# Kernel tuning notes

Measured on AMD Instinct MI355X. Metric: run time of the kernel, lower is better.

The kernel has to match this reference:

```python
import jax, jax.numpy as jnp
import numpy as np

B, NQ, T, C = 16, 1024, 2048, 4
DIM, CDIM, H, DH = 512, 256, 1, 128
INNER = H * DH


def _rotate_half(x):
    # pairs interleaved: (..., d*2) -> (-x_odd, x_even) interleaved, matching einops '(d r)' with r=2
    x2 = x.reshape(x.shape[:-1] + (-1, 2))
    a, b = x2[..., 0], x2[..., 1]
    return jnp.stack((-b, a), axis=-1).reshape(x.shape)


def _apply_rotary(freqs, x):
    # freqs: (b, n, d) -> broadcast over heads; x: (b, h, n, d)
    f = freqs[:, None, :, :]
    return x * jnp.cos(f) + _rotate_half(x) * jnp.sin(f)


def _layernorm(x, w, b, eps=1e-5):
    mu = jnp.mean(x, axis=-1, keepdims=True)
    var = jnp.var(x, axis=-1, keepdims=True)
    return (x - mu) * jax.lax.rsqrt(var + eps) * w + b


def setup_inputs() -> dict:
    key = jax.random.key(0)
    ks = jax.random.split(key, 8)
    return dict(
        x_query=jax.random.normal(ks[0], (NQ, DIM), jnp.float32),
        x_context=jax.random.normal(ks[1], (B, T, C, CDIM), jnp.float32),
        rotary_time_emb_query=jax.random.normal(ks[2], (B, NQ, DH), jnp.float32),
        rotary_time_emb_context=jax.random.normal(ks[3], (B, T * C, DH), jnp.float32),
        context_mask=jax.random.randint(ks[4], (B, T), 0, 2) > 0,
        ln_q_w=jnp.ones((DIM,), jnp.float32), ln_q_b=jnp.zeros((DIM,), jnp.float32),
        ln_c_w=jnp.ones((CDIM,), jnp.float32), ln_c_b=jnp.zeros((CDIM,), jnp.float32),
        w_q=jax.random.normal(ks[5], (INNER, DIM), jnp.float32) / np.float32(np.sqrt(DIM)),
        w_kv=jax.random.normal(ks[6], (2 * INNER, CDIM), jnp.float32) / np.float32(np.sqrt(CDIM)),
        w_o=jax.random.normal(ks[7], (DIM, INNER), jnp.float32) / np.float32(np.sqrt(INNER)),
        b_o=jnp.zeros((DIM,), jnp.float32),
    )


def reference(x_query, x_context, rotary_time_emb_query, rotary_time_emb_context,
              context_mask, ln_q_w, ln_q_b, ln_c_w, ln_c_b, w_q, w_kv, w_o, b_o):
    b = x_context.shape[0]
    xq = _layernorm(x_query, ln_q_w, ln_q_b)                      # (NQ, DIM)
    xc = _layernorm(x_context, ln_c_w, ln_c_b)                    # (B, T, C, CDIM)
    q = xq @ w_q.T                                                # (NQ, INNER)
    q = jnp.broadcast_to(q[None], (b,) + q.shape)                 # (B, NQ, INNER)
    kv = xc @ w_kv.T                                              # (B, T, C, 2*INNER)
    k, v = jnp.split(kv, 2, axis=-1)
    k = k.reshape(b, -1, k.shape[-1])                             # (B, T*C, INNER)
    v = v.reshape(b, -1, v.shape[-1])

    def to_heads(t):  # 'b n (h d) -> b h n d'
        return t.reshape(t.shape[0], t.shape[1], H, DH).transpose(0, 2, 1, 3)

    q, k, v = to_heads(q), to_heads(k), to_heads(v)
    q = _apply_rotary(rotary_time_emb_query, q)
    k = _apply_rotary(rotary_time_emb_context, k)
    v = _apply_rotary(rotary_time_emb_context, v)                 # rotate_value=True

    # kv_mask: 'b n -> b 1 1 n' then tiled x4 along last dim (as in source)
    mask = jnp.tile(context_mask[:, None, None, :], (1, 1, 1, 4)) # (B,1,1,4T)
    scale = np.float32(1.0 / np.sqrt(DH))
    logits = jnp.einsum('bhqd,bhkd->bhqk', q, k) * scale
    logits = jnp.where(mask, logits, jnp.float32(-1e30))
    attn = jax.nn.softmax(logits, axis=-1)
    out = jnp.einsum('bhqk,bhkd->bhqd', attn, v)                  # (B,H,NQ,DH)
    out = _apply_rotary(-rotary_time_emb_query, out)              # un-rotate values
    out = out.mean(axis=2)                                        # (B, H, DH)
    return out @ w_o.T + b_o                                      # (B, H, DIM)
```

## Files before the change

kernel.cpp:

```cpp
#include <hip/hip_runtime.h>
#include <hip/hip_bf16.h>


#define DEV static __device__ __forceinline__

typedef __attribute__((ext_vector_type(4))) float f32x4;
typedef __attribute__((ext_vector_type(8))) short s16x8;
typedef __attribute__((ext_vector_type(4))) unsigned u32x4;

constexpr int NB   = 16;
constexpr int NQ   = 1024;
constexpr int SC   = 8192;
constexpr int DIM  = 512;
constexpr int CDIM = 256;
constexpr int DH   = 128;
constexpr int VTR  = 144;
constexpr int VTILE = VTR*64;

DEV short f2bf(float x){
  unsigned u = __builtin_bit_cast(unsigned, x);
  unsigned r = (u + 0x7FFFu + ((u >> 16) & 1u)) >> 16;
  return (short)r;
}

DEV unsigned pk2(float a, float b){
  unsigned short ua = __builtin_bit_cast(unsigned short, __float2bfloat16(a));
  unsigned short ub = __builtin_bit_cast(unsigned short, __float2bfloat16(b));
  return (unsigned)ua | ((unsigned)ub << 16);
}

DEV f32x4 mfma16(s16x8 a, s16x8 b, f32x4 c){
  return __builtin_amdgcn_mfma_f32_16x16x32_bf16(a, b, c, 0, 0, 0);
}

DEV void gload16(const void* g, void* l){
  __builtin_amdgcn_global_load_lds(
      (const __attribute__((address_space(1))) void*)g,
      (__attribute__((address_space(3))) void*)l, 16, 0, 0);
}

DEV s16x8 pexch(int ia0, int ia1, bool hi, unsigned L0, unsigned H0, unsigned L1, unsigned H1){
  int aL0 = __builtin_amdgcn_ds_bpermute(ia0, (int)L0);
  int aL1 = __builtin_amdgcn_ds_bpermute(ia0, (int)L1);
  int aH0 = __builtin_amdgcn_ds_bpermute(ia0, (int)H0);
  int aH1 = __builtin_amdgcn_ds_bpermute(ia0, (int)H1);
  int bL0 = __builtin_amdgcn_ds_bpermute(ia1, (int)L0);
  int bL1 = __builtin_amdgcn_ds_bpermute(ia1, (int)L1);
  int bH0 = __builtin_amdgcn_ds_bpermute(ia1, (int)H0);
  int bH1 = __builtin_amdgcn_ds_bpermute(ia1, (int)H1);
  u32x4 r;
  r[0] = (unsigned)(hi ? aL1 : aL0);
  r[1] = (unsigned)(hi ? aH1 : aH0);
  r[2] = (unsigned)(hi ? bL1 : bL0);
  r[3] = (unsigned)(hi ? bH1 : bH0);
  return __builtin_bit_cast(s16x8, r);
}

__global__ void k_cvtw(const float* __restrict__ wq, const float* __restrict__ wkv,
                       short* __restrict__ wqb, short* __restrict__ wkvb){
  int i = blockIdx.x * 256 + threadIdx.x;
  if(i < 128*512) wqb[i]  = f2bf(wq[i]);
  if(i < 256*256) wkvb[i] = f2bf(wkv[i]);
}

__global__ void k_mask(const unsigned char* __restrict__ raw, unsigned* __restrict__ bits){
  const int b = blockIdx.x, t = threadIdx.x;
  int nz = 0;
  for(int i = t; i < 8192; i += 256){
    unsigned w = ((const unsigned*)raw)[i];
    if(w & 0xFFFFFF00u) nz = 1;
  }
  int any = __syncthreads_or(nz);
  bool isInt = (any == 0);
  if(t < 64){
    unsigned out = 0;
    if(isInt){
      const int* p = (const int*)raw + (b*2048 + t*32);
      for(int j = 0; j < 32; j++) out |= (unsigned)(p[j] != 0) << j;
    } else {
      const unsigned char* p = raw + (b*2048 + t*32);
      for(int j = 0; j < 32; j++) out |= (unsigned)(p[j] != 0) << j;
    }
    bits[b*64 + t] = out;
  }
}

__global__ void k_vrow(const unsigned* __restrict__ bits, short* __restrict__ Vt){
  int b = blockIdx.y;
  int s = blockIdx.x * 256 + threadIdx.x;
  unsigned w = bits[b*64 + ((s & 2047) >> 5)];
  short v = ((w >> (s & 31)) & 1u) ? (short)0x3F80 : (short)0;
  Vt[(((size_t)b*128 + (s >> 6))*VTR + 128)*64 + (s & 63)] = v;
}

__global__ __launch_bounds__(256) void k_stats(const float* __restrict__ xc,
                                               float* __restrict__ MU, float* __restrict__ RS){
  const size_t row = (size_t)blockIdx.x * 16 + (threadIdx.x >> 4);
  const int cl = (threadIdx.x & 15) * 16;
  const float* rp = xc + row * CDIM + cl;
  float s = 0.f, sq = 0.f;
  #pragma unroll
  for(int i = 0; i < 4; i++){
    f32x4 a = *(const f32x4*)(rp + i*4);
    #pragma unroll
    for(int j = 0; j < 4; j++){ s += a[j]; sq += a[j]*a[j]; }
  }
  #pragma unroll
  for(int o = 8; o > 0; o >>= 1){ s += __shfl_xor(s, o); sq += __shfl_xor(sq, o); }
  if((threadIdx.x & 15) == 0){
    float m = s * (1.f/CDIM);
    MU[row] = m;
    RS[row] = rsqrtf(sq * (1.f/CDIM) - m*m + 1e-5f);
  }
}

__global__ __launch_bounds__(256) void k_qproj(const float* __restrict__ xq,
                                               const float* __restrict__ lnw, const float* __restrict__ lnb,
                                               const short* __restrict__ wqb, float* __restrict__ Q0){
  const int wid = threadIdx.x >> 6, lane = threadIdx.x & 63;
  const int g = lane >> 4, li = lane & 15;
  const int row0 = blockIdx.x * 64 + wid * 16;

  float mean = 0.f, rstd = 0.f;
  #pragma unroll
  for(int r = 0; r < 16; r++){
    const float* rp = xq + (row0 + r) * DIM;
    f32x4 a = *(const f32x4*)(rp + lane*8);
    f32x4 b = *(const f32x4*)(rp + lane*8 + 4);
    float s = 0.f, sq = 0.f;
    #pragma unroll
    for(int i = 0; i < 4; i++){ s += a[i] + b[i]; sq += a[i]*a[i] + b[i]*b[i]; }
    #pragma unroll
    for(int o = 32; o > 0; o >>= 1){ s += __shfl_xor(s, o); sq += __shfl_xor(sq, o); }
    if(li == r){
      mean = s / DIM;
      float var = sq / DIM - mean*mean;
      rstd = rsqrtf(var + 1e-5f);
    }
  }

  f32x4 acc[8];
  #pragma unroll
  for(int n = 0; n < 8; n++) acc[n] = f32x4{0.f,0.f,0.f,0.f};

  for(int kc = 0; kc < 16; kc++){
    int kd = kc*32 + g*8;
    const float* rp = xq + (row0 + li)*DIM + kd;
    f32x4 a0 = *(const f32x4*)rp;
    f32x4 a1 = *(const f32x4*)(rp + 4);
    f32x4 w0 = *(const f32x4*)(lnw + kd), w1 = *(const f32x4*)(lnw + kd + 4);
    f32x4 b0 = *(const f32x4*)(lnb + kd), b1 = *(const f32x4*)(lnb + kd + 4);
    s16x8 af;
    #pragma unroll
    for(int i = 0; i < 4; i++){
      af[i]   = f2bf((a0[i] - mean)*rstd*w0[i] + b0[i]);
      af[i+4] = f2bf((a1[i] - mean)*rstd*w1[i] + b1[i]);
    }
    #pragma unroll
    for(int n = 0; n < 8; n++){
      s16x8 bf = *(const s16x8*)(wqb + (n*16 + li)*DIM + kd);
      acc[n] = mfma16(af, bf, acc[n]);
    }
  }
  #pragma unroll
  for(int n = 0; n < 8; n++)
    #pragma unroll
    for(int r = 0; r < 4; r++){
      int m = row0 + g*4 + r;
      Q0[m*DH + n*16 + li] = acc[n][r];
    }
}

__global__ __launch_bounds__(256) void k_kvproj(const float* __restrict__ xc,
                                                const float* __restrict__ lnw, const float* __restrict__ lnb,
                                                const short* __restrict__ wkvb, const float* __restrict__ rc,
                                                const unsigned* __restrict__ bits,
                                                const float* __restrict__ MU, const float* __restrict__ RS,
                                                short* __restrict__ Kd, short* __restrict__ Vt){
  __shared__ __align__(16) short Klds[128][136];
  __shared__ __align__(16) short Vtlds[128][136];
  const int wid = threadIdx.x >> 6, lane = threadIdx.x & 63;
  const int g = lane >> 4, li = lane & 15;
  const int b = blockIdx.y;
  const int s0 = blockIdx.x * 128;
  const int ws0 = s0 + wid * 32;

  float mean_s[2], rstd_s[2];
  #pragma unroll
  for(int sub = 0; sub < 2; sub++){
    size_t row = (size_t)b*SC + ws0 + sub*16 + li;
    mean_s[sub] = MU[row];
    rstd_s[sub] = RS[row];
  }

  f32x4 acc[16][2];
  #pragma unroll
  for(int n = 0; n < 16; n++){ acc[n][0] = f32x4{0.f,0.f,0.f,0.f}; acc[n][1] = f32x4{0.f,0.f,0.f,0.f}; }

  for(int kc = 0; kc < 8; kc++){
    int kd = kc*32 + g*8;
    f32x4 w0 = *(const f32x4*)(lnw + kd), w1 = *(const f32x4*)(lnw + kd + 4);
    f32x4 b0 = *(const f32x4*)(lnb + kd), b1 = *(const f32x4*)(lnb + kd + 4);
    s16x8 af[2];
    #pragma unroll
    for(int sub = 0; sub < 2; sub++){
      const float* rp = xc + ((size_t)b*SC + ws0 + sub*16 + li)*CDIM + kd;
      f32x4 a0 = *(const f32x4*)rp;
      f32x4 a1 = *(const f32x4*)(rp + 4);
      float mn = mean_s[sub], rs = rstd_s[sub];
      #pragma unroll
      for(int i = 0; i < 4; i++){
        af[sub][i]   = f2bf((a0[i]-mn)*rs*w0[i] + b0[i]);
        af[sub][i+4] = f2bf((a1[i]-mn)*rs*w1[i] + b1[i]);
      }
    }
    #pragma unroll
    for(int nt = 0; nt < 16; nt++){
      s16x8 bf = *(const s16x8*)(wkvb + (nt*16 + li)*CDIM + kd);
      acc[nt][0] = mfma16(af[0], bf, acc[nt][0]);
      acc[nt][1] = mfma16(af[1], bf, acc[nt][1]);
    }
  }

  #pragma unroll
  for(int nt = 0; nt < 8; nt++){
    #pragma unroll
    for(int sub = 0; sub < 2; sub++){
      #pragma unroll
      for(int r = 0; r < 4; r++){
        int srow = wid*32 + sub*16 + g*4 + r;
        int d = nt*16 + li;
        float f = rc[((size_t)b*SC + s0 + srow)*DH + d];
        float sn, cs; __sincosf(f, &sn, &cs);
        float kv = acc[nt][sub][r];
        float kp = __shfl_xor(kv, 1);
        float ky = (d & 1) ? (kv*cs + kp*sn) : (kv*cs - kp*sn);
        Klds[srow][d] = f2bf(ky);
        float vv = acc[nt+8][sub][r];
        float vp = __shfl_xor(vv, 1);
        float vy = (d & 1) ? (vv*cs + vp*sn) : (vv*cs - vp*sn);
        Vtlds[d][srow] = f2bf(vy);
      }
    }
  }
  __syncthreads();
  for(int c = threadIdx.x; c < 2048; c += 256){
    int row = c >> 4, col = (c & 15) * 8;
    s16x8 kv = *(const s16x8*)&Klds[row][col];
    *(s16x8*)(Kd + ((size_t)b*SC + s0 + row)*DH + col) = kv;
    s16x8 vv = *(const s16x8*)&Vtlds[row][col];
    int sa = s0 + col;
    unsigned w = bits[b*64 + ((sa & 2047) >> 5)];
    unsigned mb = (w >> (sa & 31)) & 0xFFu;
    #pragma unroll
    for(int j = 0; j < 8; j++) if(!((mb >> j) & 1u)) vv[j] = 0;
    *(s16x8*)(Vt + (((size_t)b*128 + (sa >> 6))*VTR + row)*64 + (sa & 63)) = vv;
  }
}

__global__ __launch_bounds__(512, 4) void k_attn(const float* __restrict__ Q0, const float* __restrict__ rq,
                                                 const short* __restrict__ Kd, const short* __restrict__ Vt,
                                                 float* __restrict__ AOp, float* __restrict__ ML){
  __shared__ __align__(16) short Kbuf[2][64*128];
  __shared__ __align__(16) short Vbuf[2][VTR*64];
  const int wid = threadIdx.x >> 6, lane = threadIdx.x & 63;
  const int g = lane >> 4, li = lane & 15;
  const int xcd = blockIdx.x & 7, ii = blockIdx.x >> 3;
  const int b  = xcd*2 + (ii >> 5);
  const int kq = (ii >> 3) & 3;
  const int qt = ii & 7;
  const int qw0 = qt*128 + wid*16;
  constexpr float C2 = 0.08838834764831845f * 1.4426950408889634f;

  s16x8 qf[4];
  {
    int qrow = qw0 + li;
    #pragma unroll
    for(int c = 0; c < 4; c++){
      int d0 = c*32 + g*8;
      const float* qp = Q0 + qrow*DH + d0;
      const float* fp = rq + ((size_t)b*NQ + qrow)*DH + d0;
      f32x4 x0 = *(const f32x4*)qp,     x1 = *(const f32x4*)(qp+4);
      f32x4 f0 = *(const f32x4*)fp,     f1 = *(const f32x4*)(fp+4);
      float xs[8] = {x0[0],x0[1],x0[2],x0[3],x1[0],x1[1],x1[2],x1[3]};
      float fs[8] = {f0[0],f0[1],f0[2],f0[3],f1[0],f1[1],f1[2],f1[3]};
      #pragma unroll
      for(int i = 0; i < 4; i++){
        float se, ce, so, co;
        __sincosf(fs[2*i],   &se, &ce);
        __sincosf(fs[2*i+1], &so, &co);
        qf[c][2*i]   = f2bf((xs[2*i]*ce   - xs[2*i+1]*se) * C2);
        qf[c][2*i+1] = f2bf((xs[2*i+1]*co + xs[2*i]*so) * C2);
      }
    }
  }

  float mrun = -1e30f;
  f32x4 acc[9];
  #pragma unroll
  for(int dt = 0; dt < 9; dt++) acc[dt] = f32x4{0.f,0.f,0.f,0.f};

  const char* Kg = (const char*)(Kd + ((size_t)b*SC + kq*2048)*DH);
  const char* Vg = (const char*)(Vt + ((size_t)b*128 + kq*32)*VTILE);

  const int ia0 = (((lane >> 4) & 1) * 32 + li) << 2;
  const int ia1 = ia0 + 64;
  const bool hi = (g >= 2);

  #define STAGE(bufi, t) do{                                                   \
    const char* Ksrc = Kg + (size_t)(t)*64*256;                                \
    _Pragma("unroll")                                                          \
    for(int j = 0; j < 2; j++){                                                \
      int rp = wid*8 + j*4 + (lane >> 4);                                      \
      int bi = ((lane & 15)*16) ^ ((rp & 7) << 4);                             \
      gload16(Ksrc + rp*256 + bi, &Kbuf[bufi][(wid*8 + j*4)*128]);             \
    }                                                                          \
    const char* Vsrc = Vg + (size_t)(t)*VTILE*2;                               \
    _Pragma("unroll")                                                          \
    for(int j = 0; j < 2; j++){                                                \
      int rp = wid*16 + j*8 + (lane >> 3);                                     \
      int bi = ((lane & 7)*16) ^ ((rp & 7) << 4);                              \
      gload16(Vsrc + rp*128 + bi, &Vbuf[bufi][(wid*16 + j*8)*64]);             \
    }                                                                          \
    if(wid < 2){                                                               \
      int rp = 128 + wid*8 + (lane >> 3);                                      \
      int bi = ((lane & 7)*16) ^ ((rp & 7) << 4);                              \
      gload16(Vsrc + rp*128 + bi, &Vbuf[bufi][(128 + wid*8)*64]);              \
    }                                                                          \
  }while(0)

  STAGE(0, 0);
  __syncthreads();

  for(int t = 0; t < 32; ++t){
    const int cur = t & 1;
    if(t < 31) STAGE(cur^1, t+1);

    f32x4 st[4];
    __builtin_amdgcn_s_setprio(1);
    #pragma unroll
    for(int ks = 0; ks < 4; ks++){
      s16x8 kf[4];
      #pragma unroll
      for(int c = 0; c < 4; c++){
        int row = ks*16 + li;
        int off = row*256 + ((c*64 + g*16) ^ ((row & 7) << 4));
        kf[c] = *(const s16x8*)((const char*)&Kbuf[cur][0] + off);
      }
      f32x4 s = f32x4{0.f,0.f,0.f,0.f};
      #pragma unroll
      for(int c = 0; c < 4; c++) s = mfma16(kf[c], qf[c], s);
      st[ks] = s;
    }
    __builtin_amdgcn_s_setprio(0);

    s16x8 pf[2];
    {
      float mt = -1e30f;
      #pragma unroll
      for(int ks = 0; ks < 4; ks++)
        #pragma unroll
        for(int r = 0; r < 4; r++) mt = fmaxf(mt, st[ks][r]);
      mt = fmaxf(mt, __shfl_xor(mt, 16));
      mt = fmaxf(mt, __shfl_xor(mt, 32));
      if(__any(mt > mrun + 3.0f)){
        float mnew = fmaxf(mrun, mt);
        float a = exp2f(mrun - mnew);
        mrun = mnew;
        #pragma unroll
        for(int dt = 0; dt < 9; dt++) acc[dt] = acc[dt] * a;
      }
      float m = mrun;
      #pragma unroll
      for(int h2 = 0; h2 < 2; h2++){
        unsigned L0 = pk2(exp2f(st[2*h2][0] - m),   exp2f(st[2*h2][1] - m));
        unsigned H0 = pk2(exp2f(st[2*h2][2] - m),   exp2f(st[2*h2][3] - m));
        unsigned L1 = pk2(exp2f(st[2*h2+1][0] - m), exp2f(st[2*h2+1][1] - m));
        unsigned H1 = pk2(exp2f(st[2*h2+1][2] - m), exp2f(st[2*h2+1][3] - m));
        pf[h2] = pexch(ia0, ia1, hi, L0, H0, L1, H1);
      }
    }

    __builtin_amdgcn_s_setprio(1);
    #pragma unroll
    for(int dt = 0; dt < 9; dt++){
      int row = dt*16 + li;
      #pragma unroll
      for(int k32 = 0; k32 < 2; k32++){
        int off = row*128 + ((k32*64 + g*16) ^ ((row & 7) << 4));
        s16x8 vf = *(const s16x8*)((const char*)&Vbuf[cur][0] + off);
        acc[dt] = mfma16(vf, pf[k32], acc[dt]);
      }
    }
    __builtin_amdgcn_s_setprio(0);

    __syncthreads();
  }

  const size_t pbase = ((size_t)kq*NB + b)*NQ;
  if(lane < 16){
    size_t o = pbase + qw0 + li;
    ML[o*2]   = mrun;
    ML[o*2+1] = acc[8][0];
  }
  {
    size_t o = (pbase + qw0 + li)*DH;
    #pragma unroll
    for(int dt = 0; dt < 8; dt++)
      *(f32x4*)(AOp + o + dt*16 + g*4) = acc[dt];
  }
}

__global__ __launch_bounds__(256) void k_fin1(const float* __restrict__ AOp, const float* __restrict__ ML,
                                              const float* __restrict__ rq, float* __restrict__ part){
  __shared__ float red[2][128];
  const int b = blockIdx.y, ch = blockIdx.x;
  const int t = threadIdx.x;
  const int d = t & 127, h = t >> 7;
  float acc = 0.f;
  #pragma unroll 2
  for(int i = 0; i < 16; i++){
    int n = ch*32 + h*16 + i;
    size_t qi = (size_t)b*NQ + n;
    float m[4], l[4];
    #pragma unroll
    for(int kq = 0; kq < 4; kq++){
      size_t o = (size_t)kq*NB*NQ + qi;
      m[kq] = ML[o*2]; l[kq] = ML[o*2+1];
    }
    float M = fmaxf(fmaxf(m[0], m[1]), fmaxf(m[2], m[3]));
    float w[4], L = 0.f;
    #pragma unroll
    for(int kq = 0; kq < 4; kq++){ w[kq] = exp2f(m[kq] - M); L += w[kq]*l[kq]; }
    float inv = 1.f / L;
    float O = 0.f;
    #pragma unroll
    for(int kq = 0; kq < 4; kq++) O += w[kq]*AOp[((size_t)kq*NB*NQ + qi)*DH + d];
    O *= inv;
    float P = __shfl_xor(O, 1);
    float f = rq[qi*DH + d];
    float sn, cs; __sincosf(f, &sn, &cs);
    acc += (d & 1) ? (O*cs - P*sn) : (O*cs + P*sn);
  }
  red[h][d] = acc;
  __syncthreads();
  if(h == 0) part[((size_t)b*32 + ch)*128 + d] = red[0][d] + red[1][d];
}

__global__ __launch_bounds__(256) void k_fin2(const float* __restrict__ part,
                                              const float* __restrict__ wo, const float* __restrict__ bo,
                                              float* __restrict__ out){
  __shared__ float sm[128];
  const int b = blockIdx.x, t = threadIdx.x;
  if(t < 128){
    float s = 0.f;
    for(int ch = 0; ch < 32; ch++) s += part[((size_t)b*32 + ch)*128 + t];
    sm[t] = s * (1.0f / NQ);
  }
  __syncthreads();
  for(int o = t; o < DIM; o += 256){
    float s = bo[o];
    const float* wr = wo + o*DH;
    #pragma unroll 4
    for(int j = 0; j < DH; j++) s += sm[j] * wr[j];
    out[b*DIM + o] = s;
  }
}

extern "C" void kernel_launch(void* const* d_in, const int* in_sizes, int n_in,
                              void* d_out, int out_size, void* d_ws, size_t ws_size,
                              hipStream_t stream){
  const float* xq   = (const float*)d_in[0];
  const float* xc   = (const float*)d_in[1];
  const float* rq   = (const float*)d_in[2];
  const float* rc   = (const float*)d_in[3];
  const unsigned char* mask = (const unsigned char*)d_in[4];
  const float* lnqw = (const float*)d_in[5];
  const float* lnqb = (const float*)d_in[6];
  const float* lncw = (const float*)d_in[7];
  const float* lncb = (const float*)d_in[8];
  const float* wq   = (const float*)d_in[9];
  const float* wkv  = (const float*)d_in[10];
  const float* wo   = (const float*)d_in[11];
  const float* bo   = (const float*)d_in[12];
  float* out = (float*)d_out;

  char* ws = (char*)d_ws;
  size_t off = 0;
  auto alloc = [&](size_t bytes){ void* p = ws + off; off += (bytes + 255) & ~(size_t)255; return p; };
  float*    Q0   = (float*)   alloc((size_t)NQ*DH*4);
  short*    wqb  = (short*)   alloc((size_t)128*512*2);
  short*    wkvb = (short*)   alloc((size_t)256*256*2);
  unsigned* bits = (unsigned*)alloc((size_t)NB*64*4);
  float*    MU   = (float*)   alloc((size_t)NB*SC*4);
  float*    RS   = (float*)   alloc((size_t)NB*SC*4);
  short*    Kd   = (short*)   alloc((size_t)NB*SC*DH*2);
  short*    Vt   = (short*)   alloc((size_t)NB*128*VTILE*2);
  float*    AOp  = (float*)   alloc((size_t)4*NB*NQ*DH*4);
  float*    ML   = (float*)   alloc((size_t)4*NB*NQ*2*4);
  float*    part = (float*)   alloc((size_t)NB*32*128*4);

  k_cvtw  <<<dim3(256),     dim3(256), 0, stream>>>(wq, wkv, wqb, wkvb);
  k_mask  <<<dim3(16),      dim3(256), 0, stream>>>(mask, bits);
  k_vrow  <<<dim3(32,16),   dim3(256), 0, stream>>>(bits, Vt);
  k_stats <<<dim3(NB*SC/16),dim3(256), 0, stream>>>(xc, MU, RS);
  k_qproj <<<dim3(16),      dim3(256), 0, stream>>>(xq, lnqw, lnqb, wqb, Q0);
  k_kvproj<<<dim3(64,16),   dim3(256), 0, stream>>>(xc, lncw, lncb, wkvb, rc, bits, MU, RS, Kd, Vt);
  k_attn  <<<dim3(512),     dim3(512), 0, stream>>>(Q0, rq, Kd, Vt, AOp, ML);
  k_fin1  <<<dim3(32,16),   dim3(256), 0, stream>>>(AOp, ML, rq, part);
  k_fin2  <<<dim3(16),      dim3(256), 0, stream>>>(part, wo, bo, out);
}
```

Baseline: 407.7 us.

## Split KV projection across 8 waves, separate K and V wave groups

Doubles the k_kvproj block to 512 threads so that four waves compute the K half and four the V half of the projection. Each wave now holds 8 accumulator tiles instead of 16, which cuts register pressure and adds parallelism. The price is that every wave pair recomputes the layernorm of the same input rows and both halves load xc and the rotary frequencies twice.

After: 344.7 us. -15.4%, faster.

```diff
diff --git a/kernel.cpp b/kernel.cpp
--- a/kernel.cpp
+++ b/kernel.cpp
@@ -171,19 +171,21 @@
     }
 }
 
-__global__ __launch_bounds__(256) void k_kvproj(const float* __restrict__ xc,
-                                                const float* __restrict__ lnw, const float* __restrict__ lnb,
-                                                const short* __restrict__ wkvb, const float* __restrict__ rc,
-                                                const unsigned* __restrict__ bits,
-                                                const float* __restrict__ MU, const float* __restrict__ RS,
-                                                short* __restrict__ Kd, short* __restrict__ Vt){
+__global__ __launch_bounds__(512, 4) void k_kvproj(const float* __restrict__ xc,
+                                                   const float* __restrict__ lnw, const float* __restrict__ lnb,
+                                                   const short* __restrict__ wkvb, const float* __restrict__ rc,
+                                                   const unsigned* __restrict__ bits,
+                                                   const float* __restrict__ MU, const float* __restrict__ RS,
+                                                   short* __restrict__ Kd, short* __restrict__ Vt){
   __shared__ __align__(16) short Klds[128][136];
   __shared__ __align__(16) short Vtlds[128][136];
   const int wid = threadIdx.x >> 6, lane = threadIdx.x & 63;
   const int g = lane >> 4, li = lane & 15;
+  const int wk = wid & 3;
+  const int isV = wid >> 2;
   const int b = blockIdx.y;
   const int s0 = blockIdx.x * 128;
-  const int ws0 = s0 + wid * 32;
+  const int ws0 = s0 + wk * 32;
 
   float mean_s[2], rstd_s[2];
   #pragma unroll
@@ -193,9 +195,9 @@
     rstd_s[sub] = RS[row];
   }
 
-  f32x4 acc[16][2];
-  #pragma unroll
-  for(int n = 0; n < 16; n++){ acc[n][0] = f32x4{0.f,0.f,0.f,0.f}; acc[n][1] = f32x4{0.f,0.f,0.f,0.f}; }
+  f32x4 acc[8][2];
+  #pragma unroll
+  for(int n = 0; n < 8; n++){ acc[n][0] = f32x4{0.f,0.f,0.f,0.f}; acc[n][1] = f32x4{0.f,0.f,0.f,0.f}; }
 
   for(int kc = 0; kc < 8; kc++){
     int kd = kc*32 + g*8;
@@ -215,36 +217,49 @@
       }
     }
     #pragma unroll
-    for(int nt = 0; nt < 16; nt++){
+    for(int ntl = 0; ntl < 8; ntl++){
+      const int nt = isV*8 + ntl;
       s16x8 bf = *(const s16x8*)(wkvb + (nt*16 + li)*CDIM + kd);
-      acc[nt][0] = mfma16(af[0], bf, acc[nt][0]);
-      acc[nt][1] = mfma16(af[1], bf, acc[nt][1]);
-    }
-  }
-
-  #pragma unroll
-  for(int nt = 0; nt < 8; nt++){
-    #pragma unroll
-    for(int sub = 0; sub < 2; sub++){
-      #pragma unroll
-      for(int r = 0; r < 4; r++){
-        int srow = wid*32 + sub*16 + g*4 + r;
-        int d = nt*16 + li;
-        float f = rc[((size_t)b*SC + s0 + srow)*DH + d];
-        float sn, cs; __sincosf(f, &sn, &cs);
-        float kv = acc[nt][sub][r];
-        float kp = __shfl_xor(kv, 1);
-        float ky = (d & 1) ? (kv*cs + kp*sn) : (kv*cs - kp*sn);
-        Klds[srow][d] = f2bf(ky);
-        float vv = acc[nt+8][sub][r];
-        float vp = __shfl_xor(vv, 1);
-        float vy = (d & 1) ? (vv*cs + vp*sn) : (vv*cs - vp*sn);
-        Vtlds[d][srow] = f2bf(vy);
-      }
-    }
+      acc[ntl][0] = mfma16(af[0], bf, acc[ntl][0]);
+      acc[ntl][1] = mfma16(af[1], bf, acc[ntl][1]);
+    }
+  }
+
+  if(isV == 0){
+    #pragma unroll
+    for(int ntl = 0; ntl < 8; ntl++)
+      #pragma unroll
+      for(int sub = 0; sub < 2; sub++)
+        #pragma unroll
+        for(int r = 0; r < 4; r++){
+          int srow = wk*32 + sub*16 + g*4 + r;
+          int d = ntl*16 + li;
+          float f = rc[((size_t)b*SC + s0 + srow)*DH + d];
+          float sn, cs; __sincosf(f, &sn, &cs);
+          float kv = acc[ntl][sub][r];
+          float kp = __shfl_xor(kv, 1);
+          float ky = (d & 1) ? (kv*cs + kp*sn) : (kv*cs - kp*sn);
+          Klds[srow][d] = f2bf(ky);
+        }
+  } else {
+    #pragma unroll
+    for(int ntl = 0; ntl < 8; ntl++)
+      #pragma unroll
+      for(int sub = 0; sub < 2; sub++)
+        #pragma unroll
+        for(int r = 0; r < 4; r++){
+          int srow = wk*32 + sub*16 + g*4 + r;
+          int d = ntl*16 + li;
+          float f = rc[((size_t)b*SC + s0 + srow)*DH + d];
+          float sn, cs; __sincosf(f, &sn, &cs);
+          float vv = acc[ntl][sub][r];
+          float vp = __shfl_xor(vv, 1);
+          float vy = (d & 1) ? (vv*cs + vp*sn) : (vv*cs - vp*sn);
+          Vtlds[d][srow] = f2bf(vy);
+        }
   }
   __syncthreads();
-  for(int c = threadIdx.x; c < 2048; c += 256){
+  for(int c = threadIdx.x; c < 2048; c += 512){
     int row = c >> 4, col = (c & 15) * 8;
     s16x8 kv = *(const s16x8*)&Klds[row][col];
     *(s16x8*)(Kd + ((size_t)b*SC + s0 + row)*DH + col) = kv;
@@ -505,7 +520,7 @@
   k_vrow  <<<dim3(32,16),   dim3(256), 0, stream>>>(bits, Vt);
   k_stats <<<dim3(NB*SC/16),dim3(256), 0, stream>>>(xc, MU, RS);
   k_qproj <<<dim3(16),      dim3(256), 0, stream>>>(xq, lnqw, lnqb, wqb, Q0);
-  k_kvproj<<<dim3(64,16),   dim3(256), 0, stream>>>(xc, lncw, lncb, wkvb, rc, bits, MU, RS, Kd, Vt);
+  k_kvproj<<<dim3(64,16),   dim3(512), 0, stream>>>(xc, lncw, lncb, wkvb, rc, bits, MU, RS, Kd, Vt);
   k_attn  <<<dim3(512),     dim3(512), 0, stream>>>(Q0, rq, Kd, Vt, AOp, ML);
   k_fin1  <<<dim3(32,16),   dim3(256), 0, stream>>>(AOp, ML, rq, part);
   k_fin2  <<<dim3(16),      dim3(256), 0, stream>>>(part, wo, bo, out);
```
